# Kernel tuning notes

Measured on AMD Instinct MI355X. Metric: run time of the kernel, lower is better.

Reference implementation:

```python
import jax, jax.numpy as jnp
import numpy as np

DEPTH, DIM, HEADS, SEQ, BATCH = 4, 512, 8, 4096, 2
DH = DIM // HEADS
BUCKET = 64          # blindspot_size -> bucket size of causal linear attention
FF = 4 * DIM
EPS_ATTN = 1e-3
EPS_LN = 1e-5


def layer_norm(x, g, b):
    mu = jnp.mean(x, axis=-1, keepdims=True)
    var = jnp.mean(jnp.square(x - mu), axis=-1, keepdims=True)
    return (x - mu) * jax.lax.rsqrt(var + EPS_LN) * g + b


def causal_linear_attn(q, k, v, bucket_size=BUCKET, eps=EPS_ATTN):
    # q,k,v: [b,h,n,e]; kernelized causal attention with bucketed cumsums
    b, h, n, e = q.shape
    q = jax.nn.softmax(q, axis=-1) * (e ** -0.5)
    k = jnp.exp(k)
    bucket = lambda t: t.reshape(b, h, n // bucket_size, bucket_size, e)
    b_q, b_k, b_v = bucket(q), bucket(k), bucket(v)
    # running sums of keys per bucket: [b,h,u,e]
    b_k_cumsum = jnp.cumsum(b_k.sum(axis=-2), axis=-2)
    # cumulative outer-product context: [b,h,u,d,e]
    context = jnp.cumsum(jnp.einsum('bhund,bhune->bhude', b_k, b_v), axis=2)
    if bucket_size > 1:
        # shift by one bucket: queries in bucket u see only buckets < u (blindspot)
        context = jnp.pad(context, ((0, 0), (0, 0), (1, 0), (0, 0), (0, 0)))[:, :, :-1]
        b_k_cumsum = jnp.pad(b_k_cumsum, ((0, 0), (0, 0), (1, 0), (0, 0)))[:, :, :-1]
    D = jnp.einsum('bhud,bhund->bhun', b_k_cumsum, b_q)
    D_inv = 1.0 / jnp.clip(D, eps, None)
    out = jnp.einsum('bhund,bhude,bhun->bhune', b_q, context, D_inv)
    return out.reshape(b, h, n, e)


def setup_inputs() -> dict:
    key = jax.random.key(0)
    ks = jax.random.split(key, 10)
    s = 0.02
    f32 = jnp.float32
    return {
        'x': jax.random.normal(ks[0], (BATCH, SEQ, DIM), f32),
        'ln1_g': jnp.ones((DEPTH, DIM), f32),
        'ln1_b': jnp.zeros((DEPTH, DIM), f32),
        'wq': jax.random.normal(ks[1], (DEPTH, DIM, DIM), f32) * s,
        'wk': jax.random.normal(ks[2], (DEPTH, DIM, DIM), f32) * s,
        'wv': jax.random.normal(ks[3], (DEPTH, DIM, DIM), f32) * s,
        'wo': jax.random.normal(ks[4], (DEPTH, DIM, DIM), f32) * s,
        'bo': jnp.zeros((DEPTH, DIM), f32),
        'ln2_g': jnp.ones((DEPTH, DIM), f32),
        'ln2_b': jnp.zeros((DEPTH, DIM), f32),
        'w1': jax.random.normal(ks[5], (DEPTH, DIM, FF), f32) * s,
        'b1': jnp.zeros((DEPTH, FF), f32),
        'w2': jax.random.normal(ks[6], (DEPTH, FF, DIM), f32) * s,
        'b2': jnp.zeros((DEPTH, DIM), f32),
    }


def reference(x, ln1_g, ln1_b, wq, wk, wv, wo, bo, ln2_g, ln2_b, w1, b1, w2, b2):
    b, n, d = x.shape
    split = lambda t: t.reshape(b, n, HEADS, DH).transpose(0, 2, 1, 3)  # [b,h,n,dh]
    for i in range(DEPTH):
        # PreNorm(SelfAttention) with residual
        h = layer_norm(x, ln1_g[i], ln1_b[i])
        q, k, v = split(h @ wq[i]), split(h @ wk[i]), split(h @ wv[i])
        att = causal_linear_attn(q, k, v)
        att = att.transpose(0, 2, 1, 3).reshape(b, n, d)
        x = x + (att @ wo[i] + bo[i])
        # PreNorm(FeedForward) with residual (GELU, no GLU)
        h = layer_norm(x, ln2_g[i], ln2_b[i])
        x = x + (jax.nn.gelu(h @ w1[i] + b1[i], approximate=False) @ w2[i] + b2[i])
    return x
```

## Files before the change

### kernel.cpp

```cpp
#include <hip/hip_runtime.h>

typedef unsigned short u16;
typedef __bf16 bf16x8 __attribute__((ext_vector_type(8)));
typedef float floatx4 __attribute__((ext_vector_type(4)));

#define DIM 512
#define HEADS 8
#define DH 64
#define SEQ 4096
#define BATCH 2
#define ROWS (BATCH * SEQ)
#define FFDIM 2048
#define QKVW 1536
#define LSTRIDE 3145728L
#define GK 512

#define SBAR0() __builtin_amdgcn_sched_barrier(0)
#define ASM_VMCNT(n) asm volatile("s_waitcnt vmcnt(" #n ")" ::: "memory")

__device__ __forceinline__ float b2f(u16 u) {
  union { float f; unsigned int i; } c; c.i = ((unsigned int)u) << 16; return c.f;
}
__device__ __forceinline__ u16 f2b(float f) {
  union { float f; unsigned int i; } c; c.f = f;
  unsigned int r = c.i + 0x7FFFu + ((c.i >> 16) & 1u);
  return (u16)(r >> 16);
}
__device__ __forceinline__ float ldin(const void* p, long i, int bf) {
  return bf ? b2f(((const u16*)p)[i]) : ((const float*)p)[i];
}
__device__ __forceinline__ void ld16(const u16* g, u16* l) {
  __builtin_amdgcn_global_load_lds((const __attribute__((address_space(1))) void*)g,
                                   (__attribute__((address_space(3))) void*)l, 16, 0, 0);
}
__device__ __forceinline__ void unpk8(uint4 p, float* o) {
  o[0] = b2f((u16)(p.x & 0xFFFF)); o[1] = b2f((u16)(p.x >> 16));
  o[2] = b2f((u16)(p.y & 0xFFFF)); o[3] = b2f((u16)(p.y >> 16));
  o[4] = b2f((u16)(p.z & 0xFFFF)); o[5] = b2f((u16)(p.z >> 16));
  o[6] = b2f((u16)(p.w & 0xFFFF)); o[7] = b2f((u16)(p.w >> 16));
}
__device__ __forceinline__ float fast_gelu(float v) {
  float z = fabsf(v) * 0.70710678118654752f;
  float t = 1.0f / (1.0f + 0.3275911f * z);
  float p = t * (0.254829592f +
           t * (-0.284496736f +
           t * (1.421413741f +
           t * (-1.453152027f +
           t * 1.061405429f))));
  float e = __expf(-z * z);
  float er = 1.0f - p * e;
  float s = copysignf(er, v);
  return 0.5f * v * (1.0f + s);
}

__global__ void k_detect(const void* __restrict__ g, int* __restrict__ flag) {
  *flag = (((const u16*)g)[0] == 0x3F80u) ? 1 : 0;
}

__global__ __launch_bounds__(256) void k_x2f(const void* __restrict__ in, float* __restrict__ out,
                                             int n, const int* __restrict__ dt) {
  int bf = *dt;
  int i = blockIdx.x * 256 + threadIdx.x;
  if (i < n) out[i] = ldin(in, i, bf);
}
__global__ __launch_bounds__(256) void k_store(const float* __restrict__ in, void* __restrict__ out,
                                               int n, const int* __restrict__ dt) {
  int bf = *dt;
  int i = blockIdx.x * 256 + threadIdx.x;
  if (i < n) {
    if (bf) ((u16*)out)[i] = f2b(in[i]);
    else ((float*)out)[i] = in[i];
  }
}

__device__ __forceinline__ void repack_tile(const void* W, long w_off, u16* R, int N,
                                            int n16tot, int j_off, int kb, int jb, int bf) {
  int t = threadIdx.x;
  __shared__ float tile[32][65];
  int r0 = t >> 6;
  int c = t & 63;
#pragma unroll
  for (int i = 0; i < 8; ++i) {
    int rr = i * 4 + r0;
    tile[rr][c] = ldin(W, w_off + (long)(kb * 32 + rr) * N + jb * 64 + c, bf);
  }
  __syncthreads();
  int lane = t & 63, w = t >> 6;
  alignas(16) u16 tmp[8];
#pragma unroll
  for (int r = 0; r < 8; ++r) tmp[r] = f2b(tile[(lane >> 4) * 8 + r][w * 16 + (lane & 15)]);
  long oidx = (((long)kb * n16tot + j_off + jb * 4 + w) * 64 + lane) * 8;
  *(uint4*)(R + oidx) = *(const uint4*)tmp;
}
__global__ __launch_bounds__(256) void k_repackQ(const void* wq, const void* wk,
                                                 const void* wv, const void* wo,
                                                 u16* WR, const int* __restrict__ dt) {
  int bf = *dt;
  int z = blockIdx.z, layer = z >> 2, type = z & 3;
  const void* W = (type == 0) ? wq : (type == 1) ? wk : (type == 2) ? wv : wo;
  u16* R = WR + (long)layer * LSTRIDE + (type < 3 ? 0 : 786432);
  int n16tot = (type < 3) ? 96 : 32;
  int j_off = (type < 3) ? type * 32 : 0;
  repack_tile(W, (long)layer * 262144, R, 512, n16tot, j_off, blockIdx.x, blockIdx.y, bf);
}
__global__ __launch_bounds__(256) void k_repackF1(const void* w1, u16* WR, const int* __restrict__ dt) {
  int bf = *dt;
  repack_tile(w1, (long)blockIdx.z * 1048576, WR + (long)blockIdx.z * LSTRIDE + 1048576,
              2048, 128, 0, blockIdx.x, blockIdx.y, bf);
}
__global__ __launch_bounds__(256) void k_repackF2(const void* w2, u16* WR, const int* __restrict__ dt) {
  int bf = *dt;
  repack_tile(w2, (long)blockIdx.z * 1048576, WR + (long)blockIdx.z * LSTRIDE + 2097152,
              512, 32, 0, blockIdx.x, blockIdx.y, bf);
}

__global__ __launch_bounds__(256) void k_ln(const float* __restrict__ x,
                                            const void* __restrict__ g, const void* __restrict__ b,
                                            long gb_off, u16* __restrict__ out,
                                            const int* __restrict__ dt) {
  int bf = *dt;
  int row = blockIdx.x;
  int t = threadIdx.x;
  const float* xr = x + (size_t)row * DIM;
  float v0 = xr[t], v1 = xr[t + 256];
  float s = v0 + v1;
  float s2 = v0 * v0 + v1 * v1;
#pragma unroll
  for (int off = 32; off > 0; off >>= 1) {
    s += __shfl_down(s, off);
    s2 += __shfl_down(s2, off);
  }
  __shared__ float red[8];
  int lane = t & 63, w = t >> 6;
  if (lane == 0) { red[w] = s; red[4 + w] = s2; }
  __syncthreads();
  float ts = red[0] + red[1] + red[2] + red[3];
  float ts2 = red[4] + red[5] + red[6] + red[7];
  float mean = ts * (1.0f / DIM);
  float var = ts2 * (1.0f / DIM) - mean * mean;
  float rstd = rsqrtf(var + 1e-5f);
  u16* orow = out + (size_t)row * DIM;
  orow[t] = f2b((v0 - mean) * rstd * ldin(g, gb_off + t, bf) + ldin(b, gb_off + t, bf));
  orow[t + 256] = f2b((v1 - mean) * rstd * ldin(g, gb_off + t + 256, bf) + ldin(b, gb_off + t + 256, bf));
}

template <int TK>
__global__ __launch_bounds__(256) void k_gemm3(const u16* __restrict__ A, const u16* __restrict__ BR,
                                               const void* bias, long bias_off,
                                               const float* __restrict__ res, float* __restrict__ outp,
                                               const int* __restrict__ dtflag) {
  constexpr int NKT = TK >> 6;
  int lane = threadIdx.x & 63;
  int wid = threadIdx.x >> 6;
  int wm = wid & 1, wn = wid >> 1;
  int m0 = blockIdx.x * 128;
  int n0 = blockIdx.y * 64;
  int n016 = blockIdx.y * 4;
  constexpr int N16 = 32;

  constexpr int BUFB = 24 * 1024;
  __shared__ alignas(16) char smem[2 * BUFB];

  floatx4 acc[4][2];
#pragma unroll
  for (int mi = 0; mi < 4; ++mi)
#pragma unroll
    for (int j = 0; j < 2; ++j)
#pragma unroll
      for (int r = 0; r < 4; ++r) acc[mi][j][r] = 0.0f;

  int arow = lane >> 3;
  int acu = ((lane & 7) ^ arow) * 8;
  const u16* AgS = A + (size_t)(m0 + wid * 32 + arow) * TK + acu;

  auto stage = [&](int kb, int b) {
    u16* aL = (u16*)(smem + b * BUFB);
    u16* bL = aL + 8192;
#pragma unroll
    for (int j = 0; j < 4; ++j)
      ld16(AgS + (size_t)(j * 8) * TK + (size_t)kb * 64, aL + (wid * 4 + j) * 512);
    ld16(BR + (((size_t)(kb * 2) * N16 + n016 + wid) * 64 + lane) * 8, bL + wid * 512);
    ld16(BR + (((size_t)(kb * 2 + 1) * N16 + n016 + wid) * 64 + lane) * 8, bL + 2048 + wid * 512);
  };

  int aoff = (lane & 15) * 64;
  int axor = (lane & 7) << 3;
  int ak0 = ((lane >> 4) * 8) ^ axor;
  int ak1 = (32 + (lane >> 4) * 8) ^ axor;

  stage(0, 0);
  stage(1, 1);
  ASM_VMCNT(6);
  __builtin_amdgcn_s_barrier();
  SBAR0();

#pragma unroll
  for (int kb = 0; kb < NKT; ++kb) {
    const u16* aL = (const u16*)(smem + (kb & 1) * BUFB);
    const u16* bL = aL + 8192;
#pragma unroll
    for (int h = 0; h < 2; ++h) {
      int akh = h ? ak1 : ak0;
      bf16x8 afr[4], bfr[2];
#pragma unroll
      for (int mi = 0; mi < 4; ++mi)
        afr[mi] = *(const bf16x8*)(aL + (wm * 4 + mi) * 1024 + aoff + akh);
#pragma unroll
      for (int j = 0; j < 2; ++j)
        bfr[j] = *(const bf16x8*)(bL + h * 2048 + ((wn * 2 + j) * 64 + lane) * 8);
      __builtin_amdgcn_s_setprio(1);
#pragma unroll
      for (int mi = 0; mi < 4; ++mi)
#pragma unroll
        for (int j = 0; j < 2; ++j)
          acc[mi][j] = __builtin_amdgcn_mfma_f32_16x16x32_bf16(afr[mi], bfr[j], acc[mi][j], 0, 0, 0);
      __builtin_amdgcn_s_setprio(0);
    }
    SBAR0();
    __builtin_amdgcn_s_barrier();
    if (kb + 2 < NKT) {
      stage(kb + 2, kb & 1);
      ASM_VMCNT(6);
    } else if (kb + 1 < NKT) {
      ASM_VMCNT(0);
    }
    __builtin_amdgcn_s_barrier();
    SBAR0();
  }

  float* epf = (float*)smem + wid * 2048;
  int dtv = *dtflag;
  int nW = n0 + wn * 32;
  int mWb = m0 + wm * 64;
  float bv[2];
#pragma unroll
  for (int j = 0; j < 2; ++j)
    bv[j] = ldin(bias, bias_off + nW + j * 16 + (lane & 15), dtv);
#pragma unroll
  for (int mi = 0; mi < 4; ++mi)
#pragma unroll
    for (int j = 0; j < 2; ++j)
#pragma unroll
      for (int r = 0; r < 4; ++r) {
        int row = mi * 16 + (lane >> 4) * 4 + r;
        int s = (row >> 2) & 3;
        int col = (j * 16 + (lane & 15)) ^ (s << 2);
        epf[row * 32 + col] = acc[mi][j][r] + bv[j];
      }
  asm volatile("s_waitcnt lgkmcnt(0)" ::: "memory");
#pragma unroll
  for (int p = 0; p < 8; ++p) {
    int row = p * 8 + (lane >> 3);
    int s = (row >> 2) & 3;
    int g = (lane & 7) ^ s;
    float4 v = *(const float4*)(epf + row * 32 + g * 4);
    size_t gi = (size_t)(mWb + row) * DIM + nW + (lane & 7) * 4;
    float4 rv = *(const float4*)&res[gi];
    v.x += rv.x; v.y += rv.y; v.z += rv.z; v.w += rv.w;
    *(float4*)&outp[gi] = v;
  }
}

template <bool HAS_BIAS, bool DO_GELU, int NN>
__device__ __forceinline__ void gemm8_body(const u16* __restrict__ A, const u16* __restrict__ BR,
                                           const void* bias, long bias_off,
                                           u16* __restrict__ outp,
                                           const int* __restrict__ dtflag) {
  constexpr int NKT = GK >> 6;
  constexpr int N16 = NN >> 4;
  int lane = threadIdx.x & 63;
  int w = threadIdx.x >> 6;
  int wm = w >> 2, wn = w & 3;
  int m0 = blockIdx.x * 256;
  int n0 = blockIdx.y * 256;
  int n016 = blockIdx.y * 16;

  __shared__ alignas(16) u16 smem8[65536];

  int arow = lane >> 3;
  int acu = ((lane & 7) ^ arow) * 8;
  const u16* Ag0 = A + (size_t)(m0 + (w * 2 + 0) * 8 + arow) * GK + acu;
  const u16* Ag1 = A + (size_t)(m0 + (w * 2 + 1) * 8 + arow) * GK + acu;
  const u16* Bg = BR + (size_t)n016 * 512 + lane * 8;

  auto stage_full = [&](int kt, int dbuf) {
    u16* aD = smem8 + dbuf * 32768;
    u16* bD = aD + 16384;
    size_t go = (size_t)kt * 64;
#pragma unroll
    for (int half = 0; half < 2; ++half) {
      ld16(Ag0 + (size_t)half * 128 * GK + go, aD + half * 8192 + (w * 2 + 0) * 512);
      ld16(Ag1 + (size_t)half * 128 * GK + go, aD + half * 8192 + (w * 2 + 1) * 512);
    }
#pragma unroll
    for (int kk = 0; kk < 2; ++kk) {
      const u16* s = Bg + ((size_t)(kt * 2 + kk) * N16) * 512;
      ld16(s + (size_t)w * 512,       bD + kk * 8192 + (0 + w) * 512);
      ld16(s + (size_t)(8 + w) * 512, bD + kk * 8192 + (8 + w) * 512);
    }
  };

  int aoff = (lane & 15) * 64;
  int axor = (lane & 7) << 3;
  int ak0 = ((lane >> 4) * 8) ^ axor;
  int ak1 = (32 + (lane >> 4) * 8) ^ axor;

  floatx4 acc[8][4];
#pragma unroll
  for (int mi = 0; mi < 8; ++mi)
#pragma unroll
    for (int j = 0; j < 4; ++j)
#pragma unroll
      for (int r = 0; r < 4; ++r) acc[mi][j][r] = 0.0f;

  stage_full(0, 0);
  stage_full(1, 1);
  ASM_VMCNT(8);
  __builtin_amdgcn_s_barrier();
  SBAR0();

#pragma unroll
  for (int c = 0; c < NKT; ++c) {
    const u16* aL = smem8 + (c & 1) * 32768;
    const u16* bL = aL + 16384;
#pragma unroll
    for (int kk = 0; kk < 2; ++kk) {
      int akh = kk ? ak1 : ak0;
      bf16x8 bfr[4];
#pragma unroll
      for (int i = 0; i < 4; ++i)
        bfr[i] = *(const bf16x8*)(bL + ((kk * 16 + wn * 4 + i) * 64 + lane) * 8);
#pragma unroll
      for (int mh = 0; mh < 2; ++mh) {
        bf16x8 afr[4];
#pragma unroll
        for (int i = 0; i < 4; ++i)
          afr[i] = *(const bf16x8*)(aL + (wm * 8 + mh * 4 + i) * 1024 + aoff + akh);
        __builtin_amdgcn_s_setprio(1);
#pragma unroll
        for (int mi = 0; mi < 4; ++mi)
#pragma unroll
          for (int j = 0; j < 4; ++j)
            acc[mh * 4 + mi][j] =
                __builtin_amdgcn_mfma_f32_16x16x32_bf16(afr[mi], bfr[j], acc[mh * 4 + mi][j], 0, 0, 0);
        __builtin_amdgcn_s_setprio(0);
      }
    }
    SBAR0();
    __builtin_amdgcn_s_barrier();
    if (c + 2 < NKT) {
      stage_full(c + 2, c & 1);
      ASM_VMCNT(8);
    } else if (c + 1 < NKT) {
      ASM_VMCNT(0);
    }
    __builtin_amdgcn_s_barrier();
    SBAR0();
  }

  ASM_VMCNT(0);
  __builtin_amdgcn_s_barrier();

  u16* epw = smem8 + w * 8192;
  int dtv = HAS_BIAS ? *dtflag : 0;
  int nW = n0 + wn * 64;
  int mW = m0 + wm * 128;
  float bv[4];
#pragma unroll
  for (int j = 0; j < 4; ++j)
    bv[j] = HAS_BIAS ? ldin(bias, bias_off + nW + j * 16 + (lane & 15), dtv) : 0.0f;
#pragma unroll
  for (int mf = 0; mf < 8; ++mf)
#pragma unroll
    for (int j = 0; j < 4; ++j)
#pragma unroll
      for (int r = 0; r < 4; ++r) {
        float v = acc[mf][j][r] + bv[j];
        if (DO_GELU) v = fast_gelu(v);
        int row = mf * 16 + (lane >> 4) * 4 + r;
        int s = (row >> 2) & 3;
        int col = (j * 16 + (lane & 15)) ^ (s << 3);
        epw[row * 64 + col] = f2b(v);
      }
  asm volatile("s_waitcnt lgkmcnt(0)" ::: "memory");
#pragma unroll
  for (int p = 0; p < 16; ++p) {
    int row = p * 8 + (lane >> 3);
    int s = (row >> 2) & 3;
    int g = (lane & 7) ^ s;
    uint4 pk = *(const uint4*)(epw + row * 64 + g * 8);
    size_t gi = (size_t)(mW + row) * NN + nW + (lane & 7) * 8;
    *(uint4*)&outp[gi] = pk;
  }
}

__global__ __launch_bounds__(512, 2) void k_g8a(const u16* __restrict__ A, const u16* __restrict__ BR,
                                                u16* __restrict__ outp, const int* dtflag) {
  gemm8_body<false, false, QKVW>(A, BR, nullptr, 0, outp, dtflag);
}
__global__ __launch_bounds__(512, 2) void k_g8b(const u16* __restrict__ A, const u16* __restrict__ BR,
                                                const void* bias, long bias_off,
                                                u16* __restrict__ outp, const int* dtflag) {
  gemm8_body<true, true, FFDIM>(A, BR, bias, bias_off, outp, dtflag);
}

__global__ __launch_bounds__(256) void k_attnA(const u16* __restrict__ qkv,
                                               float* __restrict__ Ksum, float* __restrict__ KV) {
  int u = blockIdx.x & 63;
  int bh = blockIdx.x >> 6;
  int head = bh & 7, batch = bh >> 3;
  int t = threadIdx.x;
  int pr = t >> 2, s = t & 3;
  __shared__ float kex[64][68];
  __shared__ float vv[64][68];
  const u16* base = qkv + (size_t)(batch * SEQ + u * 64 + pr) * QKVW + head * DH;
  uint4 kp0 = *(const uint4*)(base + 512 + s * 16);
  uint4 kp1 = *(const uint4*)(base + 512 + s * 16 + 8);
  uint4 vp0 = *(const uint4*)(base + 1024 + s * 16);
  uint4 vp1 = *(const uint4*)(base + 1024 + s * 16 + 8);
  float kf[16], vf[16];
  unpk8(kp0, kf); unpk8(kp1, kf + 8);
  unpk8(vp0, vf); unpk8(vp1, vf + 8);
#pragma unroll
  for (int i = 0; i < 16; ++i) {
    kex[pr][s * 16 + i] = expf(fminf(kf[i], 30.0f));
    vv[pr][s * 16 + i] = vf[i];
  }
  __syncthreads();
  int d = pr;
  float acc[16];
#pragma unroll
  for (int i = 0; i < 16; ++i) acc[i] = 0.0f;
  float ks = 0.0f;
  for (int p = 0; p < 64; ++p) {
    float kp = kex[p][d];
    ks += kp;
#pragma unroll
    for (int i4 = 0; i4 < 4; ++i4) {
      float4 v4 = *(const float4*)&vv[p][s * 16 + i4 * 4];
      acc[i4 * 4 + 0] += kp * v4.x;
      acc[i4 * 4 + 1] += kp * v4.y;
      acc[i4 * 4 + 2] += kp * v4.z;
      acc[i4 * 4 + 3] += kp * v4.w;
    }
  }
  float* kvout = KV + (size_t)blockIdx.x * 4096 + d * 64 + s * 16;
#pragma unroll
  for (int i4 = 0; i4 < 4; ++i4) {
    float4 o; o.x = acc[i4 * 4]; o.y = acc[i4 * 4 + 1]; o.z = acc[i4 * 4 + 2]; o.w = acc[i4 * 4 + 3];
    *(float4*)(kvout + i4 * 4) = o;
  }
  if (s == 0) Ksum[(size_t)blockIdx.x * 64 + d] = ks;
}

__global__ __launch_bounds__(64) void k_scan2(float* __restrict__ Ksum, float* __restrict__ KV) {
  int bh = blockIdx.x >> 6;
  int d = blockIdx.x & 63;
  int e = threadIdx.x;
  float* p0 = KV + (size_t)bh * 64 * 4096 + d * 64 + e;
  float v[64];
#pragma unroll
  for (int u = 0; u < 64; ++u) v[u] = p0[(size_t)u * 4096];
  float run = 0.0f;
#pragma unroll
  for (int u = 0; u < 64; ++u) { float c = v[u]; v[u] = run; run += c; }
#pragma unroll
  for (int u = 0; u < 64; ++u) p0[(size_t)u * 4096] = v[u];
  if (d == 0) {
    float* kp = Ksum + (size_t)bh * 4096 + e;
    float sv[64];
#pragma unroll
    for (int u = 0; u < 64; ++u) sv[u] = kp[u * 64];
    float r = 0.0f;
#pragma unroll
    for (int u = 0; u < 64; ++u) { float c = sv[u]; sv[u] = r; r += c; }
#pragma unroll
    for (int u = 0; u < 64; ++u) kp[u * 64] = sv[u];
  }
}

__global__ __launch_bounds__(256) void k_attnC(const u16* __restrict__ qkv, const float* __restrict__ Ksum,
                                               const float* __restrict__ KV, u16* __restrict__ att) {
  int u = blockIdx.x & 63;
  int bh = blockIdx.x >> 6;
  int head = bh & 7, batch = bh >> 3;
  int t = threadIdx.x;
  int pos = t >> 2, s = t & 3;
  __shared__ float Cm[64][68];
  __shared__ float qs[64][68];
  __shared__ float S[64];
  const float* kvb = KV + (size_t)blockIdx.x * 4096 + pos * 64 + s * 16;
#pragma unroll
  for (int i4 = 0; i4 < 4; ++i4)
    *(float4*)&Cm[pos][s * 16 + i4 * 4] = *(const float4*)(kvb + i4 * 4);
  if (t < 64) S[t] = Ksum[(size_t)blockIdx.x * 64 + t];
  size_t grow = (size_t)(batch * SEQ + u * 64 + pos) * QKVW + head * DH;
  uint4 q0 = *(const uint4*)(qkv + grow + s * 16);
  uint4 q1 = *(const uint4*)(qkv + grow + s * 16 + 8);
  float q[16];
  unpk8(q0, q); unpk8(q1, q + 8);
  float mx = q[0];
#pragma unroll
  for (int i = 1; i < 16; ++i) mx = fmaxf(mx, q[i]);
  mx = fmaxf(mx, __shfl_xor(mx, 1));
  mx = fmaxf(mx, __shfl_xor(mx, 2));
  float sum = 0.0f;
#pragma unroll
  for (int i = 0; i < 16; ++i) { q[i] = expf(q[i] - mx); sum += q[i]; }
  sum += __shfl_xor(sum, 1);
  sum += __shfl_xor(sum, 2);
  float scale = 0.125f / sum;
  __syncthreads();
  float Dp = 0.0f;
#pragma unroll
  for (int i = 0; i < 16; ++i) { q[i] *= scale; Dp += q[i] * S[s * 16 + i]; }
  Dp += __shfl_xor(Dp, 1);
  Dp += __shfl_xor(Dp, 2);
  float Dinv = 1.0f / fmaxf(Dp, 1e-3f);
#pragma unroll
  for (int i = 0; i < 16; ++i) qs[pos][s * 16 + i] = q[i];
  __syncthreads();
  float o[16];
#pragma unroll
  for (int i = 0; i < 16; ++i) o[i] = 0.0f;
  for (int d = 0; d < 64; ++d) {
    float qd = qs[pos][d];
#pragma unroll
    for (int i4 = 0; i4 < 4; ++i4) {
      float4 c4 = *(const float4*)&Cm[d][s * 16 + i4 * 4];
      o[i4 * 4 + 0] += qd * c4.x;
      o[i4 * 4 + 1] += qd * c4.y;
      o[i4 * 4 + 2] += qd * c4.z;
      o[i4 * 4 + 3] += qd * c4.w;
    }
  }
  u16* orow = att + (size_t)(batch * SEQ + u * 64 + pos) * DIM + head * DH + s * 16;
  uint4 pk0, pk1;
  pk0.x = (unsigned)f2b(o[0] * Dinv) | ((unsigned)f2b(o[1] * Dinv) << 16);
  pk0.y = (unsigned)f2b(o[2] * Dinv) | ((unsigned)f2b(o[3] * Dinv) << 16);
  pk0.z = (unsigned)f2b(o[4] * Dinv) | ((unsigned)f2b(o[5] * Dinv) << 16);
  pk0.w = (unsigned)f2b(o[6] * Dinv) | ((unsigned)f2b(o[7] * Dinv) << 16);
  pk1.x = (unsigned)f2b(o[8] * Dinv) | ((unsigned)f2b(o[9] * Dinv) << 16);
  pk1.y = (unsigned)f2b(o[10] * Dinv) | ((unsigned)f2b(o[11] * Dinv) << 16);
  pk1.z = (unsigned)f2b(o[12] * Dinv) | ((unsigned)f2b(o[13] * Dinv) << 16);
  pk1.w = (unsigned)f2b(o[14] * Dinv) | ((unsigned)f2b(o[15] * Dinv) << 16);
  *(uint4*)orow = pk0;
  *(uint4*)(orow + 8) = pk1;
}

extern "C" void kernel_launch(void* const* d_in, const int* in_sizes, int n_in,
                              void* d_out, int out_size, void* d_ws, size_t ws_size,
                              hipStream_t stream) {
  (void)in_sizes; (void)n_in; (void)out_size; (void)ws_size;
  const void* x_in = d_in[0];
  const void* ln1_g = d_in[1];
  const void* ln1_b = d_in[2];
  const void* wq = d_in[3];
  const void* wk = d_in[4];
  const void* wv = d_in[5];
  const void* wo = d_in[6];
  const void* bo = d_in[7];
  const void* ln2_g = d_in[8];
  const void* ln2_b = d_in[9];
  const void* w1 = d_in[10];
  const void* b1 = d_in[11];
  const void* w2 = d_in[12];
  const void* b2 = d_in[13];

  char* ws = (char*)d_ws;
  float* xf = (float*)(ws);
  u16* h = (u16*)(ws + 16777216);
  u16* region = (u16*)(ws + 25165824);
  float* Ksum = (float*)(ws + 58720256);
  float* KV = (float*)(ws + 58982400);
  u16* WR = (u16*)(ws + 75759616);
  int* dt = (int*)(ws + 100925440);
  u16* qkv = region;
  u16* gb = region;

  auto WqkvR = [&](int i) { return WR + (size_t)i * LSTRIDE + 0; };
  auto WoR   = [&](int i) { return WR + (size_t)i * LSTRIDE + 786432; };
  auto W1R   = [&](int i) { return WR + (size_t)i * LSTRIDE + 1048576; };
  auto W2R   = [&](int i) { return WR + (size_t)i * LSTRIDE + 2097152; };

  k_detect<<<dim3(1), dim3(1), 0, stream>>>(ln1_g, dt);

  const int nx = ROWS * DIM;
  k_x2f<<<dim3((nx + 255) / 256), dim3(256), 0, stream>>>(x_in, xf, nx, dt);

  k_repackQ<<<dim3(16, 8, 16), dim3(256), 0, stream>>>(wq, wk, wv, wo, WR, dt);
  k_repackF1<<<dim3(16, 32, 4), dim3(256), 0, stream>>>(w1, WR, dt);
  k_repackF2<<<dim3(64, 8, 4), dim3(256), 0, stream>>>(w2, WR, dt);

  for (int i = 0; i < 4; ++i) {
    k_ln<<<dim3(ROWS), dim3(256), 0, stream>>>(xf, ln1_g, ln1_b, (long)i * DIM, h, dt);
    k_g8a<<<dim3(32, 6), dim3(512), 0, stream>>>(h, WqkvR(i), qkv, dt);
    k_attnA<<<dim3(1024), dim3(256), 0, stream>>>(qkv, Ksum, KV);
    k_scan2<<<dim3(1024), dim3(64), 0, stream>>>(Ksum, KV);
    k_attnC<<<dim3(1024), dim3(256), 0, stream>>>(qkv, Ksum, KV, h);
    k_gemm3<512><<<dim3(64, 8), dim3(256), 0, stream>>>(h, WoR(i), bo, (long)i * DIM, xf, xf, dt);
    k_ln<<<dim3(ROWS), dim3(256), 0, stream>>>(xf, ln2_g, ln2_b, (long)i * DIM, h, dt);
    k_g8b<<<dim3(32, 8), dim3(512), 0, stream>>>(h, W1R(i), b1, (long)i * FFDIM, gb, dt);
    k_gemm3<2048><<<dim3(64, 8), dim3(256), 0, stream>>>(gb, W2R(i), b2, (long)i * DIM, xf, xf, dt);
  }

  k_store<<<dim3((nx + 255) / 256), dim3(256), 0, stream>>>(xf, d_out, nx, dt);
}
```

Baseline: 761.6 us.

## Use bf16 MFMA for per-bucket KV outer products and query-context products

Replaces the scalar fp32 FMA loops in the attention bucket kernels (k_attnA computing K^T V per bucket, k_attnC computing q·context) with 16x16x32 bf16 MFMA instructions. Operands are staged in LDS as bf16 in transposed, XOR-swizzled layouts, which halves shared-memory footprint and avoids bank conflicts. The context matrix and queries are rounded to bf16, which lowers precision relative to the fp32 path. Output stores become narrower scattered 2-byte writes rather than 16-byte vector stores.

```diff
diff --git a/kernel.cpp b/kernel.cpp
--- a/kernel.cpp
+++ b/kernel.cpp
@@ -410,47 +410,70 @@
   int bh = blockIdx.x >> 6;
   int head = bh & 7, batch = bh >> 3;
   int t = threadIdx.x;
-  int pr = t >> 2, s = t & 3;
-  __shared__ float kex[64][68];
-  __shared__ float vv[64][68];
-  const u16* base = qkv + (size_t)(batch * SEQ + u * 64 + pr) * QKVW + head * DH;
-  uint4 kp0 = *(const uint4*)(base + 512 + s * 16);
-  uint4 kp1 = *(const uint4*)(base + 512 + s * 16 + 8);
-  uint4 vp0 = *(const uint4*)(base + 1024 + s * 16);
-  uint4 vp1 = *(const uint4*)(base + 1024 + s * 16 + 8);
-  float kf[16], vf[16];
-  unpk8(kp0, kf); unpk8(kp1, kf + 8);
-  unpk8(vp0, vf); unpk8(vp1, vf + 8);
-#pragma unroll
-  for (int i = 0; i < 16; ++i) {
-    kex[pr][s * 16 + i] = expf(fminf(kf[i], 30.0f));
-    vv[pr][s * 16 + i] = vf[i];
+  __shared__ u16 ekt[4096];
+  __shared__ u16 vt[4096];
+  __shared__ float ks4[4][64];
+  {
+    int pr = t >> 2, s = t & 3;
+    const u16* base = qkv + (size_t)(batch * SEQ + u * 64 + pr) * QKVW + head * DH;
+    uint4 kp0 = *(const uint4*)(base + 512 + s * 16);
+    uint4 kp1 = *(const uint4*)(base + 512 + s * 16 + 8);
+    uint4 vp0 = *(const uint4*)(base + 1024 + s * 16);
+    uint4 vp1 = *(const uint4*)(base + 1024 + s * 16 + 8);
+    float kf[16];
+    unpk8(kp0, kf); unpk8(kp1, kf + 8);
+    u16 vu[16];
+    vu[0] = (u16)vp0.x; vu[1] = (u16)(vp0.x >> 16); vu[2] = (u16)vp0.y; vu[3] = (u16)(vp0.y >> 16);
+    vu[4] = (u16)vp0.z; vu[5] = (u16)(vp0.z >> 16); vu[6] = (u16)vp0.w; vu[7] = (u16)(vp0.w >> 16);
+    vu[8] = (u16)vp1.x; vu[9] = (u16)(vp1.x >> 16); vu[10] = (u16)vp1.y; vu[11] = (u16)(vp1.y >> 16);
+    vu[12] = (u16)vp1.z; vu[13] = (u16)(vp1.z >> 16); vu[14] = (u16)vp1.w; vu[15] = (u16)(vp1.w >> 16);
+#pragma unroll
+    for (int i = 0; i < 16; ++i) {
+      int row = s * 16 + i;
+      int col = pr ^ ((i & 7) << 3);
+      ekt[row * 64 + col] = f2b(expf(fminf(kf[i], 30.0f)));
+      vt[row * 64 + col] = vu[i];
+    }
   }
   __syncthreads();
-  int d = pr;
-  float acc[16];
-#pragma unroll
-  for (int i = 0; i < 16; ++i) acc[i] = 0.0f;
-  float ks = 0.0f;
-  for (int p = 0; p < 64; ++p) {
-    float kp = kex[p][d];
-    ks += kp;
-#pragma unroll
-    for (int i4 = 0; i4 < 4; ++i4) {
-      float4 v4 = *(const float4*)&vv[p][s * 16 + i4 * 4];
-      acc[i4 * 4 + 0] += kp * v4.x;
-      acc[i4 * 4 + 1] += kp * v4.y;
-      acc[i4 * 4 + 2] += kp * v4.z;
-      acc[i4 * 4 + 3] += kp * v4.w;
-    }
-  }
-  float* kvout = KV + (size_t)blockIdx.x * 4096 + d * 64 + s * 16;
-#pragma unroll
-  for (int i4 = 0; i4 < 4; ++i4) {
-    float4 o; o.x = acc[i4 * 4]; o.y = acc[i4 * 4 + 1]; o.z = acc[i4 * 4 + 2]; o.w = acc[i4 * 4 + 3];
-    *(float4*)(kvout + i4 * 4) = o;
-  }
-  if (s == 0) Ksum[(size_t)blockIdx.x * 64 + d] = ks;
+  int w = t >> 6, l = t & 63;
+  int X = (l & 7) << 3;
+  {
+    uint4 e0 = *(const uint4*)(ekt + l * 64 + ((w * 16) ^ X));
+    uint4 e1 = *(const uint4*)(ekt + l * 64 + ((w * 16 + 8) ^ X));
+    float f0[8], f1[8];
+    unpk8(e0, f0); unpk8(e1, f1);
+    float ssum = 0.0f;
+#pragma unroll
+    for (int i = 0; i < 8; ++i) ssum += f0[i] + f1[i];
+    ks4[w][l] = ssum;
+  }
+  floatx4 acc[4];
+#pragma unroll
+  for (int nf = 0; nf < 4; ++nf)
+#pragma unroll
+    for (int r = 0; r < 4; ++r) acc[nf][r] = 0.0f;
+  int dl = w * 16 + (l & 15);
+#pragma unroll
+  for (int kc = 0; kc < 2; ++kc) {
+    int poff = kc * 32 + (l >> 4) * 8;
+    bf16x8 afr = *(const bf16x8*)(ekt + dl * 64 + (poff ^ X));
+#pragma unroll
+    for (int nf = 0; nf < 4; ++nf) {
+      bf16x8 bfr = *(const bf16x8*)(vt + (nf * 16 + (l & 15)) * 64 + (poff ^ X));
+      acc[nf] = __builtin_amdgcn_mfma_f32_16x16x32_bf16(afr, bfr, acc[nf], 0, 0, 0);
+    }
+  }
+  float* kvout = KV + (size_t)blockIdx.x * 4096;
+#pragma unroll
+  for (int nf = 0; nf < 4; ++nf)
+#pragma unroll
+    for (int r = 0; r < 4; ++r) {
+      int d = w * 16 + (l >> 4) * 4 + r;
+      kvout[d * 64 + nf * 16 + (l & 15)] = acc[nf][r];
+    }
+  __syncthreads();
+  if (t < 64) Ksum[(size_t)blockIdx.x * 64 + t] = ks4[0][t] + ks4[1][t] + ks4[2][t] + ks4[3][t];
 }
 
 __global__ __launch_bounds__(64) void k_scan2(float* __restrict__ Ksum, float* __restrict__ KV) {
@@ -486,13 +509,22 @@
   int head = bh & 7, batch = bh >> 3;
   int t = threadIdx.x;
   int pos = t >> 2, s = t & 3;
-  __shared__ float Cm[64][68];
-  __shared__ float qs[64][68];
+  __shared__ u16 cmt[4096];
+  __shared__ u16 qst[4096];
   __shared__ float S[64];
-  const float* kvb = KV + (size_t)blockIdx.x * 4096 + pos * 64 + s * 16;
-#pragma unroll
-  for (int i4 = 0; i4 < 4; ++i4)
-    *(float4*)&Cm[pos][s * 16 + i4 * 4] = *(const float4*)(kvb + i4 * 4);
+  __shared__ float dinv[64];
+  {
+    const float* kvb = KV + (size_t)blockIdx.x * 4096 + pos * 64 + s * 16;
+    float cf[16];
+#pragma unroll
+    for (int i4 = 0; i4 < 4; ++i4) {
+      float4 c4 = *(const float4*)(kvb + i4 * 4);
+      cf[i4 * 4 + 0] = c4.x; cf[i4 * 4 + 1] = c4.y; cf[i4 * 4 + 2] = c4.z; cf[i4 * 4 + 3] = c4.w;
+    }
+#pragma unroll
+    for (int i = 0; i < 16; ++i)
+      cmt[(s * 16 + i) * 64 + (pos ^ ((i & 7) << 3))] = f2b(cf[i]);
+  }
   if (t < 64) S[t] = Ksum[(size_t)blockIdx.x * 64 + t];
   size_t grow = (size_t)(batch * SEQ + u * 64 + pos) * QKVW + head * DH;
   uint4 q0 = *(const uint4*)(qkv + grow + s * 16);
@@ -510,42 +542,57 @@
   sum += __shfl_xor(sum, 1);
   sum += __shfl_xor(sum, 2);
   float scale = 0.125f / sum;
+#pragma unroll
+  for (int i = 0; i < 16; ++i) q[i] *= scale;
+  {
+    uint4 pa, pb;
+    pa.x = (unsigned)f2b(q[0]) | ((unsigned)f2b(q[1]) << 16);
+    pa.y = (unsigned)f2b(q[2]) | ((unsigned)f2b(q[3]) << 16);
+    pa.z = (unsigned)f2b(q[4]) | ((unsigned)f2b(q[5]) << 16);
+    pa.w = (unsigned)f2b(q[6]) | ((unsigned)f2b(q[7]) << 16);
+    pb.x = (unsigned)f2b(q[8]) | ((unsigned)f2b(q[9]) << 16);
+    pb.y = (unsigned)f2b(q[10]) | ((unsigned)f2b(q[11]) << 16);
+    pb.z = (unsigned)f2b(q[12]) | ((unsigned)f2b(q[13]) << 16);
+    pb.w = (unsigned)f2b(q[14]) | ((unsigned)f2b(q[15]) << 16);
+    int Xp = (pos & 7) << 3;
+    *(uint4*)(qst + pos * 64 + ((s * 16) ^ Xp)) = pa;
+    *(uint4*)(qst + pos * 64 + ((s * 16 + 8) ^ Xp)) = pb;
+  }
   __syncthreads();
   float Dp = 0.0f;
 #pragma unroll
-  for (int i = 0; i < 16; ++i) { q[i] *= scale; Dp += q[i] * S[s * 16 + i]; }
+  for (int i = 0; i < 16; ++i) Dp += q[i] * S[s * 16 + i];
   Dp += __shfl_xor(Dp, 1);
   Dp += __shfl_xor(Dp, 2);
-  float Dinv = 1.0f / fmaxf(Dp, 1e-3f);
-#pragma unroll
-  for (int i = 0; i < 16; ++i) qs[pos][s * 16 + i] = q[i];
+  if (s == 0) dinv[pos] = 1.0f / fmaxf(Dp, 1e-3f);
+  int w = t >> 6, l = t & 63;
+  int X = (l & 7) << 3;
+  int nl = w * 16 + (l & 15);
+  floatx4 acc[4];
+#pragma unroll
+  for (int nf = 0; nf < 4; ++nf)
+#pragma unroll
+    for (int r = 0; r < 4; ++r) acc[nf][r] = 0.0f;
+#pragma unroll
+  for (int kc = 0; kc < 2; ++kc) {
+    int doff = kc * 32 + (l >> 4) * 8;
+    bf16x8 afr = *(const bf16x8*)(qst + nl * 64 + (doff ^ X));
+#pragma unroll
+    for (int nf = 0; nf < 4; ++nf) {
+      bf16x8 bfr = *(const bf16x8*)(cmt + (nf * 16 + (l & 15)) * 64 + (doff ^ X));
+      acc[nf] = __builtin_amdgcn_mfma_f32_16x16x32_bf16(afr, bfr, acc[nf], 0, 0, 0);
+    }
+  }
   __syncthreads();
-  float o[16];
-#pragma unroll
-  for (int i = 0; i < 16; ++i) o[i] = 0.0f;
-  for (int d = 0; d < 64; ++d) {
-    float qd = qs[pos][d];
-#pragma unroll
-    for (int i4 = 0; i4 < 4; ++i4) {
-      float4 c4 = *(const float4*)&Cm[d][s * 16 + i4 * 4];
-      o[i4 * 4 + 0] += qd * c4.x;
-      o[i4 * 4 + 1] += qd * c4.y;
-      o[i4 * 4 + 2] += qd * c4.z;
-      o[i4 * 4 + 3] += qd * c4.w;
-    }
-  }
-  u16* orow = att + (size_t)(batch * SEQ + u * 64 + pos) * DIM + head * DH + s * 16;
-  uint4 pk0, pk1;
-  pk0.x = (unsigned)f2b(o[0] * Dinv) | ((unsigned)f2b(o[1] * Dinv) << 16);
-  pk0.y = (unsigned)f2b(o[2] * Dinv) | ((unsigned)f2b(o[3] * Dinv) << 16);
-  pk0.z = (unsigned)f2b(o[4] * Dinv) | ((unsigned)f2b(o[5] * Dinv) << 16);
-  pk0.w = (unsigned)f2b(o[6] * Dinv) | ((unsigned)f2b(o[7] * Dinv) << 16);
-  pk1.x = (unsigned)f2b(o[8] * Dinv) | ((unsigned)f2b(o[9] * Dinv) << 16);
-  pk1.y = (unsigned)f2b(o[10] * Dinv) | ((unsigned)f2b(o[11] * Dinv) << 16);
-  pk1.z = (unsigned)f2b(o[12] * Dinv) | ((unsigned)f2b(o[13] * Dinv) << 16);
-  pk1.w = (unsigned)f2b(o[14] * Dinv) | ((unsigned)f2b(o[15] * Dinv) << 16);
-  *(uint4*)orow = pk0;
-  *(uint4*)(orow + 8) = pk1;
+  u16* ob = att + (size_t)(batch * SEQ + u * 64) * DIM + head * DH;
+#pragma unroll
+  for (int r = 0; r < 4; ++r) {
+    int n = w * 16 + (l >> 4) * 4 + r;
+    float dv = dinv[n];
+#pragma unroll
+    for (int nf = 0; nf < 4; ++nf)
+      ob[(size_t)n * DIM + nf * 16 + (l & 15)] = f2b(acc[nf][r] * dv);
+  }
 }
 
 extern "C" void kernel_launch(void* const* d_in, const int* in_sizes, int n_in,
```

Measured after the change: 665.3 us (median of 2 runs). -12.7%, faster.
